# Kernel optimization log

Hardware: AMD Instinct MI355X
Metric: run time of the kernel (lower is better)

Reference implementation:

```python
import jax, jax.numpy as jnp
import numpy as np

D_MODEL = 512
HIDDEN = 2048
NUM_EXPERTS = 8
TOP_K = 2
BATCH, SEQ = 4, 4096


def setup_inputs() -> dict:
    key = jax.random.key(0)
    kx, kg, k1, k2 = jax.random.split(key, 4)
    x = jax.random.normal(kx, (BATCH, SEQ, D_MODEL), dtype=jnp.float32)
    # gate: nn.Linear(d_model, num_experts, bias=False), init std=0.02
    Wg = 0.02 * jax.random.normal(kg, (NUM_EXPERTS, D_MODEL), dtype=jnp.float32)
    # expert weights, xavier_uniform scale
    lim1 = float(np.sqrt(6.0 / (D_MODEL + HIDDEN)))
    lim2 = float(np.sqrt(6.0 / (HIDDEN + D_MODEL)))
    W1 = jax.random.uniform(k1, (NUM_EXPERTS, D_MODEL, HIDDEN), dtype=jnp.float32, minval=-lim1, maxval=lim1)
    W2 = jax.random.uniform(k2, (NUM_EXPERTS, HIDDEN, D_MODEL), dtype=jnp.float32, minval=-lim2, maxval=lim2)
    return {"x": x, "Wg": Wg, "W1": W1, "W2": W2}


def reference(x, Wg, W1, W2):
    B, S, d = x.shape
    E = W1.shape[0]
    xf = x.reshape(-1, d)  # [T, d]
    router_logits = xf @ Wg.T  # [T, E]
    # top-k routing, softmax over selected logits
    topv, sel = jax.lax.top_k(router_logits, TOP_K)  # [T, K]
    rw = jax.nn.softmax(topv, axis=-1)  # [T, K]
    # dense combine weights [T, E]: weight for expert e if selected, else 0
    cw = jnp.sum(jax.nn.one_hot(sel, E, dtype=xf.dtype) * rw[..., None], axis=1)
    # per-expert MLP (loop over small fixed E), weighted combine
    out = jnp.zeros_like(xf)
    for e in range(E):
        h = jax.nn.gelu(xf @ W1[e], approximate=False)  # exact erf GELU like nn.GELU
        out = out + cw[:, e:e + 1] * (h @ W2[e])
    return out.reshape(B, S, d), router_logits.reshape(B, S, E)
```

## Files before the change

kernel.cpp:

```cpp
#include <hip/hip_runtime.h>
#include <hip/hip_bf16.h>
#include <math.h>

#define T_TOK 16384
#define DM 512
#define HID 2048
#define NE 8

typedef unsigned short u16;
typedef unsigned long long u64;
typedef __attribute__((ext_vector_type(4))) float f32x4;
typedef __attribute__((ext_vector_type(8))) __bf16 bf16x8;

static __device__ __forceinline__ u16 f2bf(float f) {
    __hip_bfloat16 h = __float2bfloat16(f);
    union { __hip_bfloat16 h; u16 u; } c; c.h = h; return c.u;
}

static __device__ __forceinline__ bf16x8 as_bf16x8(uint4 u) {
    union { uint4 u; bf16x8 b; } c; c.u = u; return c.b;
}

__global__ __launch_bounds__(256) void cvt_x_kernel(const float* __restrict__ in,
                                                    u16* __restrict__ out) {
    int i = blockIdx.x * 256 + threadIdx.x;
    const float4* p = (const float4*)in + (size_t)i * 2;
    float4 a = p[0], b = p[1];
    union { u16 s[8]; uint4 v; } r;
    r.s[0] = f2bf(a.x); r.s[1] = f2bf(a.y); r.s[2] = f2bf(a.z); r.s[3] = f2bf(a.w);
    r.s[4] = f2bf(b.x); r.s[5] = f2bf(b.y); r.s[6] = f2bf(b.z); r.s[7] = f2bf(b.w);
    *((uint4*)out + i) = r.v;
}

__global__ __launch_bounds__(256) void transpose_cvt(const float* __restrict__ in,
                                                     u16* __restrict__ out, int R, int C) {
    __shared__ float tile[32][33];
    const float* inp = in + (size_t)blockIdx.z * R * C;
    u16* outp = out + (size_t)blockIdx.z * R * C;
    int c0 = blockIdx.x * 32, r0 = blockIdx.y * 32;
    for (int i = threadIdx.y; i < 32; i += 8)
        tile[i][threadIdx.x] = inp[(size_t)(r0 + i) * C + c0 + threadIdx.x];
    __syncthreads();
    for (int i = threadIdx.y; i < 32; i += 8)
        outp[(size_t)(c0 + i) * R + r0 + threadIdx.x] = f2bf(tile[threadIdx.x][i]);
}

__global__ __launch_bounds__(256) void router_kernel(
    const float* __restrict__ x, const float* __restrict__ Wg,
    float* __restrict__ logits, int* __restrict__ cnt,
    int* __restrict__ tlist, float* __restrict__ wlist)
{
    __shared__ int   s_sel[128];
    __shared__ float s_w[128];
    const int wave = threadIdx.x >> 6, lane = threadIdx.x & 63;
    const int tbase = blockIdx.x * 64;

    for (int i = 0; i < 16; i++) {
        int ti = wave * 16 + i;
        int t  = tbase + ti;
        const float4* xp = (const float4*)(x + (size_t)t * DM) + lane * 2;
        float4 a0 = xp[0], a1 = xp[1];
        float acc[NE];
#pragma unroll
        for (int e = 0; e < NE; e++) {
            const float4* wp = (const float4*)(Wg + e * DM) + lane * 2;
            float4 b0 = wp[0], b1 = wp[1];
            acc[e] = a0.x*b0.x + a0.y*b0.y + a0.z*b0.z + a0.w*b0.w
                   + a1.x*b1.x + a1.y*b1.y + a1.z*b1.z + a1.w*b1.w;
        }
#pragma unroll
        for (int e = 0; e < NE; e++) {
#pragma unroll
            for (int off = 32; off >= 1; off >>= 1)
                acc[e] += __shfl_xor(acc[e], off, 64);
        }
        if (lane == 0) {
            float4* lg = (float4*)(logits + (size_t)t * NE);
            lg[0] = make_float4(acc[0], acc[1], acc[2], acc[3]);
            lg[1] = make_float4(acc[4], acc[5], acc[6], acc[7]);
            int i0 = 0; float v0 = acc[0];
#pragma unroll
            for (int e = 1; e < NE; e++) if (acc[e] > v0) { v0 = acc[e]; i0 = e; }
            int i1 = -1; float v1 = -1e30f;
#pragma unroll
            for (int e = 0; e < NE; e++) if (e != i0 && acc[e] > v1) { v1 = acc[e]; i1 = e; }
            float w0 = 1.f / (1.f + __expf(v1 - v0) * 0.f + expf(v1 - v0));
            s_sel[ti * 2] = i0; s_sel[ti * 2 + 1] = i1;
            s_w[ti * 2] = w0;   s_w[ti * 2 + 1] = 1.f - w0;
        }
    }
    __syncthreads();
    if (wave == 0) {
        int s0 = s_sel[lane * 2], s1 = s_sel[lane * 2 + 1];
        float w0 = s_w[lane * 2], w1 = s_w[lane * 2 + 1];
        u64 A = 0, B = 0, C = 0;
        int myTot = 0;
#pragma unroll
        for (int e = 0; e < NE; e++) {
            u64 q0 = __ballot(s0 == e);
            u64 q1 = __ballot(s1 == e);
            if (s0 == e) A = q0;
            if (s1 == e) { B = q0; C = q1; }
            if (lane == e) myTot = __popcll(q0) + __popcll(q1);
        }
        int base = 0;
        if (lane < NE) base = atomicAdd(&cnt[lane], myTot);
        u64 below = ((u64)1 << lane) - 1;
        int b0 = __shfl(base, s0, 64);
        int b1 = __shfl(base, s1, 64);
        int t = tbase + lane;
        int slot0 = b0 + __popcll(A & below);
        int slot1 = b1 + __popcll(B) + __popcll(C & below);
        tlist[s0 * T_TOK + slot0] = t; wlist[s0 * T_TOK + slot0] = w0;
        tlist[s1 * T_TOK + slot1] = t; wlist[s1 * T_TOK + slot1] = w1;
    }
}

__global__ __launch_bounds__(512, 2) void expert_kernel(
    const u16* __restrict__ xb, const u16* __restrict__ W1T, const u16* __restrict__ W2T,
    const int* __restrict__ cnt, const int* __restrict__ tlist, const float* __restrict__ wlist,
    float* __restrict__ out)
{
    const int e = blockIdx.y;
    const int n = cnt[e];
    const int row0 = blockIdx.x * 64;
    if (row0 >= n) return;
    const int wid = threadIdx.x >> 6;
    const int lane = threadIdx.x & 63;
    const int l15 = lane & 15, lhi = lane >> 4;

    __shared__ char xs[64 * 1024];
    __shared__ char hs[2][64 * 256];

#pragma unroll
    for (int i = 0; i < 8; i++) {
        int r = wid * 8 + i;
        int idx = row0 + r;
        int tok = (idx < n) ? tlist[e * T_TOK + idx] : 0;
        uint4 v = *(const uint4*)(xb + (size_t)tok * DM + lane * 8);
        *(uint4*)(xs + r * 1024 + ((lane * 16) ^ ((r & 7) << 4))) = v;
    }
    __syncthreads();

    f32x4 acc2[4][4];
#pragma unroll
    for (int m = 0; m < 4; m++)
#pragma unroll
        for (int nt = 0; nt < 4; nt++) acc2[m][nt] = (f32x4)0.0f;

    const u16* w1e = W1T + (size_t)e * HID * DM;
    const u16* w2e = W2T + (size_t)e * DM * HID;
    const u16* w1base = w1e + (size_t)(wid * 16 + l15) * DM + lhi * 8;
    const u16* w2base = w2e + (size_t)(wid * 64 + l15) * HID + lhi * 8;

    int xrow[4], hrow[4], swz[4];
#pragma unroll
    for (int m = 0; m < 4; m++) {
        int r = m * 16 + l15;
        xrow[m] = r * 1024;
        hrow[m] = r * 256;
        swz[m]  = (r & 7) << 4;
    }
    const int hwoff = ((wid * 32 + lhi * 8) ^ ((l15 & 7) << 4));

    for (int ch = 0; ch < HID / 128; ++ch) {
        f32x4 acc1[4];
#pragma unroll
        for (int m = 0; m < 4; m++) acc1[m] = (f32x4)0.0f;
        const u16* bp1 = w1base + (size_t)ch * 128 * DM;
#pragma unroll
        for (int ks = 0; ks < 16; ++ks) {
            bf16x8 bw1 = *(const bf16x8*)(bp1 + ks * 32);
            int colb = ks * 64 + lhi * 16;
#pragma unroll
            for (int m = 0; m < 4; ++m) {
                bf16x8 ax = *(const bf16x8*)(xs + xrow[m] + (colb ^ swz[m]));
                acc1[m] = __builtin_amdgcn_mfma_f32_16x16x32_bf16(bw1, ax, acc1[m], 0, 0, 0);
            }
        }
        uint4 bw2[16];
        const u16* bp2 = w2base + ch * 128;
#pragma unroll
        for (int nt = 0; nt < 4; ++nt)
#pragma unroll
            for (int k2 = 0; k2 < 4; ++k2)
                bw2[nt * 4 + k2] = *(const uint4*)(bp2 + (size_t)nt * 16 * HID + k2 * 32);
        char* hw = hs[ch & 1];
#pragma unroll
        for (int m = 0; m < 4; ++m) {
            union { ushort4 s; uint2 v; } pk;
            {
                float v0 = acc1[m][0], v1 = acc1[m][1], v2 = acc1[m][2], v3 = acc1[m][3];
                pk.s.x = f2bf(0.5f * v0 * (1.0f + erff(v0 * 0.70710678f)));
                pk.s.y = f2bf(0.5f * v1 * (1.0f + erff(v1 * 0.70710678f)));
                pk.s.z = f2bf(0.5f * v2 * (1.0f + erff(v2 * 0.70710678f)));
                pk.s.w = f2bf(0.5f * v3 * (1.0f + erff(v3 * 0.70710678f)));
            }
            *(uint2*)(hw + m * 16 * 256 + l15 * 256 + hwoff) = pk.v;
        }
        __syncthreads();
        const char* hr = hs[ch & 1];
#pragma unroll
        for (int k2 = 0; k2 < 4; ++k2) {
            bf16x8 a[4];
            int colb = k2 * 64 + lhi * 16;
#pragma unroll
            for (int m = 0; m < 4; ++m)
                a[m] = *(const bf16x8*)(hr + hrow[m] + (colb ^ swz[m]));
#pragma unroll
            for (int nt = 0; nt < 4; ++nt) {
                bf16x8 b = as_bf16x8(bw2[nt * 4 + k2]);
#pragma unroll
                for (int m = 0; m < 4; ++m)
                    acc2[m][nt] = __builtin_amdgcn_mfma_f32_16x16x32_bf16(a[m], b, acc2[m][nt], 0, 0, 0);
            }
        }
    }

#pragma unroll
    for (int m = 0; m < 4; m++) {
#pragma unroll
        for (int j = 0; j < 4; j++) {
            int r = m * 16 + lhi * 4 + j;
            int idx = row0 + r;
            bool ok = idx < n;
            int tok  = ok ? tlist[e * T_TOK + idx] : 0;
            float w  = ok ? wlist[e * T_TOK + idx] : 0.f;
            float* op = out + (size_t)tok * DM + wid * 64 + l15;
#pragma unroll
            for (int nt = 0; nt < 4; nt++)
                atomicAdd(op + nt * 16, acc2[m][nt][j] * w);
        }
    }
}

extern "C" void kernel_launch(void* const* d_in, const int* in_sizes, int n_in,
                              void* d_out, int out_size, void* d_ws, size_t ws_size,
                              hipStream_t stream) {
    const float* x  = (const float*)d_in[0];
    const float* Wg = (const float*)d_in[1];
    const float* W1 = (const float*)d_in[2];
    const float* W2 = (const float*)d_in[3];
    float* out = (float*)d_out;
    char* ws = (char*)d_ws;

    int*   cnt   = (int*)ws;
    int*   tlist = (int*)(ws + 1024);
    float* wlist = (float*)(ws + 1024 + NE * T_TOK * 4);
    u16*   xb    = (u16*)(ws + (2u << 20));
    u16*   W1T   = xb + (size_t)T_TOK * DM;
    u16*   W2T   = W1T + (size_t)NE * DM * HID;

    hipMemsetAsync(cnt, 0, 64, stream);
    hipMemsetAsync(out, 0, (size_t)T_TOK * DM * sizeof(float), stream);

    cvt_x_kernel<<<T_TOK * DM / 8 / 256, 256, 0, stream>>>(x, xb);
    transpose_cvt<<<dim3(HID / 32, DM / 32, NE), dim3(32, 8), 0, stream>>>(W1, W1T, DM, HID);
    transpose_cvt<<<dim3(DM / 32, HID / 32, NE), dim3(32, 8), 0, stream>>>(W2, W2T, HID, DM);
    router_kernel<<<T_TOK / 64, 256, 0, stream>>>(x, Wg, out + (size_t)T_TOK * DM,
                                                  cnt, tlist, wlist);
    expert_kernel<<<dim3(T_TOK / 64, NE), 512, 0, stream>>>(xb, W1T, W2T,
                                                            cnt, tlist, wlist, out);
}
```

Measured before the change: 642.1 us.

## Enlarge expert token tile to 128 rows, fuse x conversion into router

The expert kernel now processes 128 tokens per block. Waves are split into two token groups and four hidden groups, with 64-wide hidden chunks and a single-buffered h tile guarded by an extra barrier. Each W1/W2 weight fragment loaded from global memory is therefore reused across twice as many tokens. The grid is flattened so expert index cycles fastest, which interleaves experts across blocks. The bf16 conversion of x is fused into the router kernel, removing a separate launch and an extra read of x. The weight transpose kernel now uses 64x64 tiles with vectorised loads and stores. The trade-offs are higher register pressure from 32 accumulators per wave and extra synchronisation per chunk.

```diff
diff --git a/kernel.cpp b/kernel.cpp
--- a/kernel.cpp
+++ b/kernel.cpp
@@ -6,6 +6,9 @@
 #define DM 512
 #define HID 2048
 #define NE 8
+#define MT 128
+#define CH 64
+#define NCH (HID / CH)
 
 typedef unsigned short u16;
 typedef unsigned long long u64;
@@ -21,34 +24,36 @@
     union { uint4 u; bf16x8 b; } c; c.u = u; return c.b;
 }
 
-__global__ __launch_bounds__(256) void cvt_x_kernel(const float* __restrict__ in,
-                                                    u16* __restrict__ out) {
-    int i = blockIdx.x * 256 + threadIdx.x;
-    const float4* p = (const float4*)in + (size_t)i * 2;
-    float4 a = p[0], b = p[1];
-    union { u16 s[8]; uint4 v; } r;
-    r.s[0] = f2bf(a.x); r.s[1] = f2bf(a.y); r.s[2] = f2bf(a.z); r.s[3] = f2bf(a.w);
-    r.s[4] = f2bf(b.x); r.s[5] = f2bf(b.y); r.s[6] = f2bf(b.z); r.s[7] = f2bf(b.w);
-    *((uint4*)out + i) = r.v;
-}
-
 __global__ __launch_bounds__(256) void transpose_cvt(const float* __restrict__ in,
                                                      u16* __restrict__ out, int R, int C) {
-    __shared__ float tile[32][33];
+    __shared__ float tile[64][65];
     const float* inp = in + (size_t)blockIdx.z * R * C;
     u16* outp = out + (size_t)blockIdx.z * R * C;
-    int c0 = blockIdx.x * 32, r0 = blockIdx.y * 32;
-    for (int i = threadIdx.y; i < 32; i += 8)
-        tile[i][threadIdx.x] = inp[(size_t)(r0 + i) * C + c0 + threadIdx.x];
+    int c0 = blockIdx.x * 64, r0 = blockIdx.y * 64;
+    int tr = threadIdx.x >> 4;
+    int tc = threadIdx.x & 15;
+#pragma unroll
+    for (int i = 0; i < 4; i++) {
+        int r = i * 16 + tr;
+        float4 v = *(const float4*)(inp + (size_t)(r0 + r) * C + c0 + tc * 4);
+        tile[r][tc * 4 + 0] = v.x; tile[r][tc * 4 + 1] = v.y;
+        tile[r][tc * 4 + 2] = v.z; tile[r][tc * 4 + 3] = v.w;
+    }
     __syncthreads();
-    for (int i = threadIdx.y; i < 32; i += 8)
-        outp[(size_t)(c0 + i) * R + r0 + threadIdx.x] = f2bf(tile[threadIdx.x][i]);
+#pragma unroll
+    for (int i = 0; i < 4; i++) {
+        int c = i * 16 + tr;
+        ushort4 o;
+        o.x = f2bf(tile[tc * 4 + 0][c]); o.y = f2bf(tile[tc * 4 + 1][c]);
+        o.z = f2bf(tile[tc * 4 + 2][c]); o.w = f2bf(tile[tc * 4 + 3][c]);
+        *(ushort4*)(outp + (size_t)(c0 + c) * R + r0 + tc * 4) = o;
+    }
 }
 
 __global__ __launch_bounds__(256) void router_kernel(
     const float* __restrict__ x, const float* __restrict__ Wg,
     float* __restrict__ logits, int* __restrict__ cnt,
-    int* __restrict__ tlist, float* __restrict__ wlist)
+    int* __restrict__ tlist, float* __restrict__ wlist, u16* __restrict__ xb)
 {
     __shared__ int   s_sel[128];
     __shared__ float s_w[128];
@@ -60,6 +65,11 @@
         int t  = tbase + ti;
         const float4* xp = (const float4*)(x + (size_t)t * DM) + lane * 2;
         float4 a0 = xp[0], a1 = xp[1];
+        union { u16 s[8]; uint4 v; } px;
+        px.s[0] = f2bf(a0.x); px.s[1] = f2bf(a0.y); px.s[2] = f2bf(a0.z); px.s[3] = f2bf(a0.w);
+        px.s[4] = f2bf(a1.x); px.s[5] = f2bf(a1.y); px.s[6] = f2bf(a1.z); px.s[7] = f2bf(a1.w);
+        *(uint4*)(xb + (size_t)t * DM + lane * 8) = px.v;
+
         float acc[NE];
 #pragma unroll
         for (int e = 0; e < NE; e++) {
@@ -84,7 +94,7 @@
             int i1 = -1; float v1 = -1e30f;
 #pragma unroll
             for (int e = 0; e < NE; e++) if (e != i0 && acc[e] > v1) { v1 = acc[e]; i1 = e; }
-            float w0 = 1.f / (1.f + __expf(v1 - v0) * 0.f + expf(v1 - v0));
+            float w0 = 1.f / (1.f + expf(v1 - v0));
             s_sel[ti * 2] = i0; s_sel[ti * 2 + 1] = i1;
             s_w[ti * 2] = w0;   s_w[ti * 2 + 1] = 1.f - w0;
         }
@@ -121,20 +131,25 @@
     const int* __restrict__ cnt, const int* __restrict__ tlist, const float* __restrict__ wlist,
     float* __restrict__ out)
 {
-    const int e = blockIdx.y;
+    const int e = blockIdx.x & 7;
+    const int tile = blockIdx.x >> 3;
     const int n = cnt[e];
-    const int row0 = blockIdx.x * 64;
+    const int row0 = tile * MT;
     if (row0 >= n) return;
     const int wid = threadIdx.x >> 6;
     const int lane = threadIdx.x & 63;
     const int l15 = lane & 15, lhi = lane >> 4;
-
-    __shared__ char xs[64 * 1024];
-    __shared__ char hs[2][64 * 256];
-
-#pragma unroll
-    for (int i = 0; i < 8; i++) {
-        int r = wid * 8 + i;
+    const int tg = wid >> 2;
+    const int hg = wid & 3;
+
+    __shared__ char xs[MT * 1024];
+    __shared__ char hs[MT * CH * 2];
+
+    const int swzA = (l15 & 7) << 4;
+
+#pragma unroll
+    for (int i = 0; i < 16; i++) {
+        int r = wid * 16 + i;
         int idx = row0 + r;
         int tok = (idx < n) ? tlist[e * T_TOK + idx] : 0;
         uint4 v = *(const uint4*)(xb + (size_t)tok * DM + lane * 8);
@@ -142,94 +157,97 @@
     }
     __syncthreads();
 
-    f32x4 acc2[4][4];
-#pragma unroll
-    for (int m = 0; m < 4; m++)
+    f32x4 acc2[8][4];
+#pragma unroll
+    for (int m = 0; m < 8; m++)
 #pragma unroll
         for (int nt = 0; nt < 4; nt++) acc2[m][nt] = (f32x4)0.0f;
 
     const u16* w1e = W1T + (size_t)e * HID * DM;
     const u16* w2e = W2T + (size_t)e * DM * HID;
-    const u16* w1base = w1e + (size_t)(wid * 16 + l15) * DM + lhi * 8;
-    const u16* w2base = w2e + (size_t)(wid * 64 + l15) * HID + lhi * 8;
-
-    int xrow[4], hrow[4], swz[4];
+    const u16* w1p = w1e + (size_t)(hg * 16 + l15) * DM + lhi * 8;
+    const u16* w2p = w2e + (size_t)(wid * 64 + l15) * HID + lhi * 8;
+
+    int xbase[4], hwoff[4];
 #pragma unroll
     for (int m = 0; m < 4; m++) {
-        int r = m * 16 + l15;
-        xrow[m] = r * 1024;
-        hrow[m] = r * 256;
-        swz[m]  = (r & 7) << 4;
-    }
-    const int hwoff = ((wid * 32 + lhi * 8) ^ ((l15 & 7) << 4));
-
-    for (int ch = 0; ch < HID / 128; ++ch) {
+        int r = tg * 64 + m * 16 + l15;
+        xbase[m] = r * 1024;
+        hwoff[m] = r * (CH * 2) + ((hg * 32 + lhi * 8) ^ swzA);
+    }
+    int hbase[8];
+#pragma unroll
+    for (int m = 0; m < 8; m++) hbase[m] = (m * 16 + l15) * (CH * 2);
+
+    for (int ch = 0; ch < NCH; ++ch) {
         f32x4 acc1[4];
 #pragma unroll
         for (int m = 0; m < 4; m++) acc1[m] = (f32x4)0.0f;
-        const u16* bp1 = w1base + (size_t)ch * 128 * DM;
+        const u16* bp1 = w1p + (size_t)ch * CH * DM;
 #pragma unroll
         for (int ks = 0; ks < 16; ++ks) {
             bf16x8 bw1 = *(const bf16x8*)(bp1 + ks * 32);
             int colb = ks * 64 + lhi * 16;
 #pragma unroll
             for (int m = 0; m < 4; ++m) {
-                bf16x8 ax = *(const bf16x8*)(xs + xrow[m] + (colb ^ swz[m]));
+                bf16x8 ax = *(const bf16x8*)(xs + xbase[m] + (colb ^ swzA));
                 acc1[m] = __builtin_amdgcn_mfma_f32_16x16x32_bf16(bw1, ax, acc1[m], 0, 0, 0);
             }
         }
-        uint4 bw2[16];
-        const u16* bp2 = w2base + ch * 128;
+        uint4 bw2[8];
+        const u16* bp2 = w2p + ch * CH;
 #pragma unroll
         for (int nt = 0; nt < 4; ++nt)
 #pragma unroll
-            for (int k2 = 0; k2 < 4; ++k2)
-                bw2[nt * 4 + k2] = *(const uint4*)(bp2 + (size_t)nt * 16 * HID + k2 * 32);
-        char* hw = hs[ch & 1];
+            for (int k2 = 0; k2 < 2; ++k2)
+                bw2[nt * 2 + k2] = *(const uint4*)(bp2 + (size_t)nt * 16 * HID + k2 * 32);
+        uint2 pk[4];
 #pragma unroll
         for (int m = 0; m < 4; ++m) {
-            union { ushort4 s; uint2 v; } pk;
-            {
-                float v0 = acc1[m][0], v1 = acc1[m][1], v2 = acc1[m][2], v3 = acc1[m][3];
-                pk.s.x = f2bf(0.5f * v0 * (1.0f + erff(v0 * 0.70710678f)));
-                pk.s.y = f2bf(0.5f * v1 * (1.0f + erff(v1 * 0.70710678f)));
-                pk.s.z = f2bf(0.5f * v2 * (1.0f + erff(v2 * 0.70710678f)));
-                pk.s.w = f2bf(0.5f * v3 * (1.0f + erff(v3 * 0.70710678f)));
+            union { ushort4 s; uint2 v; } p;
+            float v0 = acc1[m][0], v1 = acc1[m][1], v2 = acc1[m][2], v3 = acc1[m][3];
+            p.s.x = f2bf(0.5f * v0 * (1.0f + erff(v0 * 0.70710678f)));
+            p.s.y = f2bf(0.5f * v1 * (1.0f + erff(v1 * 0.70710678f)));
+            p.s.z = f2bf(0.5f * v2 * (1.0f + erff(v2 * 0.70710678f)));
+            p.s.w = f2bf(0.5f * v3 * (1.0f + erff(v3 * 0.70710678f)));
+            pk[m] = p.v;
+        }
+        __syncthreads();
+#pragma unroll
+        for (int m = 0; m < 4; ++m)
+            *(uint2*)(hs + hwoff[m]) = pk[m];
+        __syncthreads();
+#pragma unroll
+        for (int k2 = 0; k2 < 2; ++k2) {
+            int colb = k2 * 64 + lhi * 16;
+            bf16x8 a2[8];
+#pragma unroll
+            for (int m = 0; m < 8; ++m)
+                a2[m] = *(const bf16x8*)(hs + hbase[m] + (colb ^ swzA));
+#pragma unroll
+            for (int nt = 0; nt < 4; ++nt) {
+                bf16x8 b = as_bf16x8(bw2[nt * 2 + k2]);
+#pragma unroll
+                for (int m = 0; m < 8; ++m)
+                    acc2[m][nt] = __builtin_amdgcn_mfma_f32_16x16x32_bf16(a2[m], b, acc2[m][nt], 0, 0, 0);
             }
-            *(uint2*)(hw + m * 16 * 256 + l15 * 256 + hwoff) = pk.v;
-        }
-        __syncthreads();
-        const char* hr = hs[ch & 1];
-#pragma unroll
-        for (int k2 = 0; k2 < 4; ++k2) {
-            bf16x8 a[4];
-            int colb = k2 * 64 + lhi * 16;
-#pragma unroll
-            for (int m = 0; m < 4; ++m)
-                a[m] = *(const bf16x8*)(hr + hrow[m] + (colb ^ swz[m]));
-#pragma unroll
-            for (int nt = 0; nt < 4; ++nt) {
-                bf16x8 b = as_bf16x8(bw2[nt * 4 + k2]);
-#pragma unroll
-                for (int m = 0; m < 4; ++m)
-                    acc2[m][nt] = __builtin_amdgcn_mfma_f32_16x16x32_bf16(a[m], b, acc2[m][nt], 0, 0, 0);
-            }
-        }
-    }
-
-#pragma unroll
-    for (int m = 0; m < 4; m++) {
-#pragma unroll
-        for (int j = 0; j < 4; j++) {
+        }
+    }
+
+#pragma unroll
+    for (int m = 0; m < 8; ++m) {
+#pragma unroll
+        for (int j = 0; j < 4; ++j) {
             int r = m * 16 + lhi * 4 + j;
             int idx = row0 + r;
-            bool ok = idx < n;
-            int tok  = ok ? tlist[e * T_TOK + idx] : 0;
-            float w  = ok ? wlist[e * T_TOK + idx] : 0.f;
-            float* op = out + (size_t)tok * DM + wid * 64 + l15;
-#pragma unroll
-            for (int nt = 0; nt < 4; nt++)
-                atomicAdd(op + nt * 16, acc2[m][nt][j] * w);
+            if (idx < n) {
+                int tok = tlist[e * T_TOK + idx];
+                float w = wlist[e * T_TOK + idx];
+                float* op = out + (size_t)tok * DM + wid * 64 + l15;
+#pragma unroll
+                for (int nt = 0; nt < 4; ++nt)
+                    atomicAdd(op + nt * 16, acc2[m][nt][j] * w);
+            }
         }
     }
 }
@@ -254,11 +272,10 @@
     hipMemsetAsync(cnt, 0, 64, stream);
     hipMemsetAsync(out, 0, (size_t)T_TOK * DM * sizeof(float), stream);
 
-    cvt_x_kernel<<<T_TOK * DM / 8 / 256, 256, 0, stream>>>(x, xb);
-    transpose_cvt<<<dim3(HID / 32, DM / 32, NE), dim3(32, 8), 0, stream>>>(W1, W1T, DM, HID);
-    transpose_cvt<<<dim3(DM / 32, HID / 32, NE), dim3(32, 8), 0, stream>>>(W2, W2T, HID, DM);
+    transpose_cvt<<<dim3(HID / 64, DM / 64, NE), 256, 0, stream>>>(W1, W1T, DM, HID);
+    transpose_cvt<<<dim3(DM / 64, HID / 64, NE), 256, 0, stream>>>(W2, W2T, HID, DM);
     router_kernel<<<T_TOK / 64, 256, 0, stream>>>(x, Wg, out + (size_t)T_TOK * DM,
-                                                  cnt, tlist, wlist);
-    expert_kernel<<<dim3(T_TOK / 64, NE), 512, 0, stream>>>(xb, W1T, W2T,
-                                                            cnt, tlist, wlist, out);
-}
+                                                  cnt, tlist, wlist, xb);
+    expert_kernel<<<(T_TOK / MT) * NE, 512, 0, stream>>>(xb, W1T, W2T,
+                                                         cnt, tlist, wlist, out);
+}
```

Result: slower. 884.8 us (+37.8%).
